# Optimization experiments

Measured on AMD Instinct MI355X. Metric: run time of the kernel, lower is better.

## Reference

```python
import jax, jax.numpy as jnp
import numpy as np

B, L, D_IN, H, N2, NL = 8, 4096, 128, 256, 8, 4  # d_state=16 -> N2=8 conjugate pairs


def setup_inputs() -> dict:
    key = jax.random.key(0)
    ks = jax.random.split(key, 10)
    x = jax.random.normal(ks[0], (B, L, D_IN), jnp.float32)
    enc_w = jax.random.normal(ks[1], (H, D_IN), jnp.float32) / np.float32(np.sqrt(D_IN))
    enc_b = jax.random.normal(ks[2], (H,), jnp.float32) * 0.01
    # S4D kernel params, stacked over NL layers
    log_dt = (jax.random.uniform(ks[3], (NL, H), jnp.float32)
              * np.float32(np.log(0.1) - np.log(0.001)) + np.float32(np.log(0.001)))
    log_A_real = jnp.full((NL, H, N2), np.float32(np.log(0.5)), jnp.float32)
    A_imag = jnp.ones((NL, H, 1), jnp.float32) * (np.pi * jnp.arange(N2, dtype=jnp.float32))
    C_re = jax.random.normal(ks[4], (NL, H, N2), jnp.float32) * np.float32(0.5 ** 0.5)
    C_im = jax.random.normal(ks[5], (NL, H, N2), jnp.float32) * np.float32(0.5 ** 0.5)
    D_skip = jax.random.normal(ks[6], (NL, H), jnp.float32)
    out_w = jax.random.normal(ks[7], (NL, 2 * H, H), jnp.float32) / np.float32(np.sqrt(H))
    out_b = jnp.zeros((NL, 2 * H), jnp.float32)
    return {"x": x, "enc_w": enc_w, "enc_b": enc_b, "log_dt": log_dt,
            "log_A_real": log_A_real, "A_imag": A_imag, "C_re": C_re, "C_im": C_im,
            "D_skip": D_skip, "out_w": out_w, "out_b": out_b}


def _s4d_layer(z, log_dt, log_A_real, A_imag, C_re, C_im, D_skip, out_w, out_b):
    # z: (B, L, H) -> u: (B, H, L)
    u = jnp.swapaxes(z, 1, 2)
    Lq = u.shape[-1]
    dt = jnp.exp(log_dt)                       # (H,)
    A = -jnp.exp(log_A_real) + 1j * A_imag     # (H, N2) complex
    dtA = A * dt[:, None]                      # (H, N2)
    Ck = (C_re + 1j * C_im) * (jnp.exp(dtA) - 1.0) / A  # ZOH discretization of C
    # Vandermonde kernel: K[h,l] = 2*Re(sum_n Ck[h,n] * exp(dtA[h,n]*l))
    t = jnp.arange(Lq, dtype=jnp.float32)
    K = 2.0 * jnp.einsum('hn,hnl->hl', Ck, jnp.exp(dtA[:, :, None] * t)).real  # (H, L)
    # FFT circular conv on 2L grid -> causal linear conv
    n_fft = 2 * Lq
    y = jnp.fft.irfft(jnp.fft.rfft(u, n=n_fft) * jnp.fft.rfft(K, n=n_fft), n=n_fft)[..., :Lq]
    y = y + u * D_skip[:, None]                # skip connection
    y = jax.nn.gelu(y)                         # final_act='gelu'
    y = jnp.einsum('bhl,ph->bpl', y, out_w) + out_b[None, :, None]  # 1x1 conv H->2H
    a, g = jnp.split(y, 2, axis=1)
    y = a * jax.nn.sigmoid(g)                  # GLU
    return jnp.swapaxes(y, 1, 2)               # (B, L, H)


def reference(x, enc_w, enc_b, log_dt, log_A_real, A_imag, C_re, C_im, D_skip, out_w, out_b):
    h = x @ enc_w.T + enc_b                    # encoder Linear: (B, L, H)
    for i in range(NL):                        # small fixed structural loop over layers
        z = _s4d_layer(h, log_dt[i], log_A_real[i], A_imag[i],
                       C_re[i], C_im[i], D_skip[i], out_w[i], out_b[i])
        h = z + h                              # residual (dropout=0 -> identity)
    return h
```

## Files before the change

### kernel.cpp

```cpp
#include <hip/hip_runtime.h>
#include <hip/hip_bf16.h>
#include <math.h>

#define Bn   8
#define Ln   4096
#define DINn 128
#define Hn   256
#define N2n  8
#define NLn  4

typedef __attribute__((ext_vector_type(4))) float f32x4;
typedef __attribute__((ext_vector_type(8))) short bf16x8;

__device__ __forceinline__ float gelu_f(float x) {
    float x2 = x * x;
    float inner = 0.7978845608028654f * x * fmaf(0.044715f, x2, 1.0f);
    float e = __expf(2.0f * inner);
    float th = 1.0f - 2.0f / (e + 1.0f);
    return 0.5f * x * (1.0f + th);
}

__device__ __forceinline__ float sigmoid_f(float x) {
    return 1.0f / (1.0f + __expf(-x));
}

__device__ __forceinline__ unsigned short f2bf(float f) {
    union { __hip_bfloat16 b; unsigned short u; } cv;
    cv.b = __float2bfloat16(f);
    return cv.u;
}

__device__ __forceinline__ uint4 pack8(float4 a, float4 b) {
    uint4 v;
    v.x = (unsigned)f2bf(a.x) | ((unsigned)f2bf(a.y) << 16);
    v.y = (unsigned)f2bf(a.z) | ((unsigned)f2bf(a.w) << 16);
    v.z = (unsigned)f2bf(b.x) | ((unsigned)f2bf(b.y) << 16);
    v.w = (unsigned)f2bf(b.z) | ((unsigned)f2bf(b.w) << 16);
    return v;
}

__global__ __launch_bounds__(256) void s4_scan_kernel(
    const float* __restrict__ hT,
    unsigned short* __restrict__ yT,
    const float* __restrict__ log_dt,
    const float* __restrict__ log_A_real,
    const float* __restrict__ A_imag,
    const float* __restrict__ C_re,
    const float* __restrict__ C_im,
    const float* __restrict__ D_skip)
{
    __shared__ float u_lds[4][64][65];
    const int tid = threadIdx.x;
    const int v = tid >> 6;
    const int t = tid & 63;
    const int h = blockIdx.x * 4 + v;
    const int b = blockIdx.y;

    const size_t rowbase = (size_t)(b * Hn + h) * Ln + (size_t)t * 64;
    const float* src = hT + rowbase;
    float* uL = &u_lds[v][t][0];

    #pragma unroll
    for (int j4 = 0; j4 < 16; ++j4) {
        float4 g = *(const float4*)(src + j4 * 4);
        uL[j4 * 4 + 0] = g.x; uL[j4 * 4 + 1] = g.y;
        uL[j4 * 4 + 2] = g.z; uL[j4 * 4 + 3] = g.w;
    }

    float dt = expf(log_dt[h]);
    float wr[N2n], wi[N2n], cr[N2n], ci[N2n];
    #pragma unroll
    for (int n = 0; n < N2n; ++n) {
        float lar = log_A_real[h * N2n + n];
        float aim = A_imag[h * N2n + n];
        float are = -expf(lar);
        float dre = are * dt, dimv = aim * dt;
        float mag = expf(dre);
        float s_, c_;
        sincosf(dimv, &s_, &c_);
        float w_re = mag * c_, w_im = mag * s_;
        wr[n] = w_re; wi[n] = w_im;
        float nre = w_re - 1.0f, nim = w_im;
        float inv = 1.0f / (are * are + aim * aim);
        float tre = (nre * are + nim * aim) * inv;
        float tim = (nim * are - nre * aim) * inv;
        float Cr = C_re[h * N2n + n], Ci = C_im[h * N2n + n];
        cr[n] = Cr * tre - Ci * tim;
        ci[n] = Cr * tim + Ci * tre;
    }
    const float Dsk = D_skip[h];

    float sr[N2n], si[N2n];
    #pragma unroll
    for (int n = 0; n < N2n; ++n) { sr[n] = 0.0f; si[n] = 0.0f; }
    #pragma unroll 4
    for (int j = 0; j < 64; ++j) {
        float u = uL[j];
        float acc = 0.0f;
        #pragma unroll
        for (int n = 0; n < N2n; ++n) {
            float nr = fmaf(wr[n], sr[n], fmaf(-wi[n], si[n], u));
            float ni = fmaf(wi[n], sr[n], wr[n] * si[n]);
            sr[n] = nr; si[n] = ni;
            acc = fmaf(cr[n], nr, fmaf(-ci[n], ni, acc));
        }
        uL[j] = fmaf(2.0f, acc, Dsk * u);
    }

    float mr[N2n], mi[N2n];
    #pragma unroll
    for (int n = 0; n < N2n; ++n) {
        float ar = wr[n], ai = wi[n];
        #pragma unroll
        for (int q = 0; q < 6; ++q) { float nr2 = ar * ar - ai * ai; ai = 2.0f * ar * ai; ar = nr2; }
        mr[n] = ar; mi[n] = ai;
    }
    for (int dlt = 1; dlt < 64; dlt <<= 1) {
        #pragma unroll
        for (int n = 0; n < N2n; ++n) {
            float tr = __shfl_up(sr[n], (unsigned)dlt, 64);
            float ti = __shfl_up(si[n], (unsigned)dlt, 64);
            float trz = (t >= dlt) ? tr : 0.0f;
            float tiz = (t >= dlt) ? ti : 0.0f;
            sr[n] = fmaf(mr[n], trz, fmaf(-mi[n], tiz, sr[n]));
            si[n] = fmaf(mr[n], tiz, fmaf(mi[n], trz, si[n]));
        }
        #pragma unroll
        for (int n = 0; n < N2n; ++n) {
            float nr2 = mr[n] * mr[n] - mi[n] * mi[n];
            mi[n] = 2.0f * mr[n] * mi[n];
            mr[n] = nr2;
        }
    }
    float pr[N2n], pim[N2n];
    #pragma unroll
    for (int n = 0; n < N2n; ++n) {
        float er = __shfl_up(sr[n], 1u, 64);
        float ei = __shfl_up(si[n], 1u, 64);
        pr[n]  = (t >= 1) ? er : 0.0f;
        pim[n] = (t >= 1) ? ei : 0.0f;
    }

    float dr2[N2n], di2[N2n];
    #pragma unroll
    for (int n = 0; n < N2n; ++n) { dr2[n] = cr[n]; di2[n] = ci[n]; }
    unsigned short* dst = yT + rowbase;
    for (int j8 = 0; j8 < 8; ++j8) {
        unsigned short rs[8];
        #pragma unroll
        for (int c = 0; c < 8; ++c) {
            float corr = 0.0f;
            #pragma unroll
            for (int n = 0; n < N2n; ++n) {
                float nr2 = dr2[n] * wr[n] - di2[n] * wi[n];
                float ni2 = dr2[n] * wi[n] + di2[n] * wr[n];
                dr2[n] = nr2; di2[n] = ni2;
                corr = fmaf(nr2, pr[n], fmaf(-ni2, pim[n], corr));
            }
            float yv = fmaf(2.0f, corr, uL[j8 * 8 + c]);
            rs[c] = f2bf(gelu_f(yv));
        }
        uint4 o;
        o.x = (unsigned)rs[0] | ((unsigned)rs[1] << 16);
        o.y = (unsigned)rs[2] | ((unsigned)rs[3] << 16);
        o.z = (unsigned)rs[4] | ((unsigned)rs[5] << 16);
        o.w = (unsigned)rs[6] | ((unsigned)rs[7] << 16);
        *(uint4*)(dst + j8 * 8) = o;
    }
}

template<int KDIM, bool GLU, bool ACVT, bool KMAJ, bool LAST>
__global__ __launch_bounds__(256) void mfma_gemm(
    const unsigned short* __restrict__ Abf,
    const float* __restrict__ Af,
    const float* __restrict__ W,
    const float* __restrict__ ba,
    const float* __restrict__ bg,
    float* hTbuf,
    float* Hout)
{
    constexpr int SM_MAIN = 128 * 72 * 2 + (GLU ? 2 : 1) * 64 * 72 * 2;
    constexpr int SM_TS = 64 * 132 * 4;
    constexpr int SM = SM_MAIN > SM_TS ? SM_MAIN : SM_TS;
    __shared__ __align__(16) char smem[SM];
    unsigned short* As  = (unsigned short*)smem;
    unsigned short* Bs0 = As + 128 * 72;
    unsigned short* Bs1 = Bs0 + 64 * 72;
    float* ts = (float*)smem;

    const int tid = threadIdx.x;
    const int lane = tid & 63, w = tid >> 6;
    const int wm = w >> 1, wn = w & 1;
    const int lr = lane & 15, lq = lane >> 4;
    const int row0 = blockIdx.x * 128;
    const int n0 = blockIdx.y * 64;
    const int bb = row0 >> 12;
    const int l0 = row0 & (Ln - 1);

    f32x4 accA[4][2], accG[4][2];
    #pragma unroll
    for (int i = 0; i < 4; ++i)
        #pragma unroll
        for (int j = 0; j < 2; ++j) {
            accA[i][j] = (f32x4)0.0f;
            if constexpr (GLU) accG[i][j] = (f32x4)0.0f;
        }

    for (int kt = 0; kt < KDIM / 64; ++kt) {
        const int k0 = kt * 64;
        if constexpr (ACVT) {
            #pragma unroll
            for (int it = 0; it < 4; ++it) {
                int idx = it * 256 + tid; int m = idx >> 3, q = idx & 7;
                const float* s = Af + (size_t)(row0 + m) * KDIM + k0 + q * 8;
                float4 g1 = *(const float4*)s;
                float4 g2 = *(const float4*)(s + 4);
                *(uint4*)(&As[m * 72 + q * 8]) = pack8(g1, g2);
            }
        } else {
            #pragma unroll
            for (int it = 0; it < 4; ++it) {
                int p = tid >> 2;
                int c = (tid & 3) | (it << 2);
                uint4 g = *(const uint4*)(Abf + (size_t)(bb * Hn + k0 + p) * Ln + l0 + c * 8);
                unsigned short* d = &As[(c * 8) * 72 + p];
                d[0 * 72] = g.x & 0xffff; d[1 * 72] = g.x >> 16;
                d[2 * 72] = g.y & 0xffff; d[3 * 72] = g.y >> 16;
                d[4 * 72] = g.z & 0xffff; d[5 * 72] = g.z >> 16;
                d[6 * 72] = g.w & 0xffff; d[7 * 72] = g.w >> 16;
            }
        }
        #pragma unroll
        for (int it = 0; it < 2; ++it) {
            int idx = it * 256 + tid; int p = idx >> 3, q = idx & 7;
            {
                const float* s = W + (size_t)(n0 + p) * KDIM + k0 + q * 8;
                float4 g1 = *(const float4*)s;
                float4 g2 = *(const float4*)(s + 4);
                *(uint4*)(&Bs0[p * 72 + q * 8]) = pack8(g1, g2);
            }
            if constexpr (GLU) {
                const float* s = W + (size_t)(256 + n0 + p) * KDIM + k0 + q * 8;
                float4 g1 = *(const float4*)s;
                float4 g2 = *(const float4*)(s + 4);
                *(uint4*)(&Bs1[p * 72 + q * 8]) = pack8(g1, g2);
            }
        }
        __syncthreads();
        #pragma unroll
        for (int kf = 0; kf < 2; ++kf) {
            bf16x8 av[4], bv[2], gv[2];
            #pragma unroll
            for (int mf = 0; mf < 4; ++mf)
                av[mf] = *(const bf16x8*)(&As[(wm * 64 + mf * 16 + lr) * 72 + (kf * 4 + lq) * 8]);
            #pragma unroll
            for (int nf = 0; nf < 2; ++nf) {
                bv[nf] = *(const bf16x8*)(&Bs0[(wn * 32 + nf * 16 + lr) * 72 + (kf * 4 + lq) * 8]);
                if constexpr (GLU)
                    gv[nf] = *(const bf16x8*)(&Bs1[(wn * 32 + nf * 16 + lr) * 72 + (kf * 4 + lq) * 8]);
            }
            #pragma unroll
            for (int mf = 0; mf < 4; ++mf)
                #pragma unroll
                for (int nf = 0; nf < 2; ++nf) {
                    accA[mf][nf] = __builtin_amdgcn_mfma_f32_16x16x32_bf16(av[mf], bv[nf], accA[mf][nf], 0, 0, 0);
                    if constexpr (GLU)
                        accG[mf][nf] = __builtin_amdgcn_mfma_f32_16x16x32_bf16(av[mf], gv[nf], accG[mf][nf], 0, 0, 0);
                }
        }
        __syncthreads();
    }

    float bA[2], bG[2];
    #pragma unroll
    for (int nf = 0; nf < 2; ++nf) {
        int pc = n0 + wn * 32 + nf * 16 + lr;
        bA[nf] = ba[pc];
        if constexpr (GLU) bG[nf] = bg[pc];
    }
    #pragma unroll
    for (int mf = 0; mf < 4; ++mf) {
        #pragma unroll
        for (int r = 0; r < 4; ++r) {
            int m_loc = wm * 64 + mf * 16 + lq * 4 + r;
            #pragma unroll
            for (int nf = 0; nf < 2; ++nf) {
                float val;
                if constexpr (GLU) {
                    float aval = accA[mf][nf][r] + bA[nf];
                    float gval = accG[mf][nf][r] + bG[nf];
                    val = aval * sigmoid_f(gval);
                } else {
                    val = accA[mf][nf][r] + bA[nf];
                }
                ts[(wn * 32 + nf * 16 + lr) * 132 + m_loc] = val;
            }
        }
    }
    __syncthreads();

    if constexpr (!LAST) {
        #pragma unroll
        for (int it2 = 0; it2 < 8; ++it2) {
            int idx = it2 * 256 + tid;
            int nn = idx >> 5, m4 = (idx & 31) * 4;
            float4 o = *(const float4*)(&ts[nn * 132 + m4]);
            float* gp = hTbuf + (size_t)(bb * Hn + n0 + nn) * Ln + l0 + m4;
            if constexpr (GLU) {
                float4 rr = *(const float4*)gp;
                o.x += rr.x; o.y += rr.y; o.z += rr.z; o.w += rr.w;
            }
            *(float4*)gp = o;
        }
    } else {
        #pragma unroll
        for (int it2 = 0; it2 < 8; ++it2) {
            int idx = it2 * 256 + tid;
            int nn = idx >> 5, m4 = (idx & 31) * 4;
            float4 o = *(const float4*)(&ts[nn * 132 + m4]);
            const float* gp = hTbuf + (size_t)(bb * Hn + n0 + nn) * Ln + l0 + m4;
            float4 rr = *(const float4*)gp;
            o.x += rr.x; o.y += rr.y; o.z += rr.z; o.w += rr.w;
            *(float4*)(&ts[nn * 132 + m4]) = o;
        }
        __syncthreads();
        #pragma unroll
        for (int it2 = 0; it2 < 8; ++it2) {
            int idx = it2 * 256 + tid;
            int m = idx >> 4, n4 = (idx & 15) * 4;
            float4 o;
            o.x = ts[(n4 + 0) * 132 + m];
            o.y = ts[(n4 + 1) * 132 + m];
            o.z = ts[(n4 + 2) * 132 + m];
            o.w = ts[(n4 + 3) * 132 + m];
            *(float4*)(Hout + (size_t)(row0 + m) * Hn + n0 + n4) = o;
        }
    }
}

extern "C" void kernel_launch(void* const* d_in, const int* in_sizes, int n_in,
                              void* d_out, int out_size, void* d_ws, size_t ws_size,
                              hipStream_t stream) {
    (void)in_sizes; (void)n_in; (void)out_size; (void)ws_size;
    const float* x          = (const float*)d_in[0];
    const float* enc_w      = (const float*)d_in[1];
    const float* enc_b      = (const float*)d_in[2];
    const float* log_dt     = (const float*)d_in[3];
    const float* log_A_real = (const float*)d_in[4];
    const float* A_imag     = (const float*)d_in[5];
    const float* C_re       = (const float*)d_in[6];
    const float* C_im       = (const float*)d_in[7];
    const float* D_skip     = (const float*)d_in[8];
    const float* out_w      = (const float*)d_in[9];
    const float* out_b      = (const float*)d_in[10];

    const size_t NE = (size_t)Bn * Hn * Ln;
    float* h  = (float*)d_out;
    float* hT = (float*)d_ws;
    unsigned short* yT = (unsigned short*)(hT + NE);

    const dim3 gg(256, 4), gb(256);

    mfma_gemm<DINn, false, true, false, false><<<gg, gb, 0, stream>>>(
        nullptr, x, enc_w, enc_b, nullptr, hT, nullptr);

    for (int i = 0; i < NLn; ++i) {
        s4_scan_kernel<<<dim3(Hn / 4, Bn), gb, 0, stream>>>(
            hT, yT,
            log_dt + (size_t)i * Hn,
            log_A_real + (size_t)i * Hn * N2n,
            A_imag + (size_t)i * Hn * N2n,
            C_re + (size_t)i * Hn * N2n,
            C_im + (size_t)i * Hn * N2n,
            D_skip + (size_t)i * Hn);
        const float* wlay = out_w + (size_t)i * 2 * Hn * Hn;
        const float* bl = out_b + (size_t)i * 2 * Hn;
        if (i == NLn - 1) {
            mfma_gemm<Hn, true, false, true, true><<<gg, gb, 0, stream>>>(
                yT, nullptr, wlay, bl, bl + Hn, hT, h);
        } else {
            mfma_gemm<Hn, true, false, true, false><<<gg, gb, 0, stream>>>(
                yT, nullptr, wlay, bl, bl + Hn, hT, nullptr);
        }
    }
}
```

Baseline: 286.8 us.

## Split each scan row across two wavefronts with cross-wave state carry

```diff
diff --git a/kernel.cpp b/kernel.cpp
--- a/kernel.cpp
+++ b/kernel.cpp
@@ -39,7 +39,7 @@
     return v;
 }
 
-__global__ __launch_bounds__(256) void s4_scan_kernel(
+__global__ __launch_bounds__(256, 4) void s4_scan_kernel(
     const float* __restrict__ hT,
     unsigned short* __restrict__ yT,
     const float* __restrict__ log_dt,
@@ -49,19 +49,23 @@
     const float* __restrict__ C_im,
     const float* __restrict__ D_skip)
 {
-    __shared__ float u_lds[4][64][65];
+    __shared__ float u_lds[2][128][33];
+    __shared__ float Sbuf[2][16];
+
     const int tid = threadIdx.x;
-    const int v = tid >> 6;
+    const int w = tid >> 6;
     const int t = tid & 63;
-    const int h = blockIdx.x * 4 + v;
+    const int rowloc = w >> 1;
+    const int half = w & 1;
+    const int h = blockIdx.x * 2 + rowloc;
     const int b = blockIdx.y;
 
-    const size_t rowbase = (size_t)(b * Hn + h) * Ln + (size_t)t * 64;
+    const size_t rowbase = (size_t)(b * Hn + h) * Ln + (size_t)half * 2048 + (size_t)t * 32;
     const float* src = hT + rowbase;
-    float* uL = &u_lds[v][t][0];
-
-    #pragma unroll
-    for (int j4 = 0; j4 < 16; ++j4) {
+    float* uL = &u_lds[rowloc][half * 64 + t][0];
+
+    #pragma unroll
+    for (int j4 = 0; j4 < 8; ++j4) {
         float4 g = *(const float4*)(src + j4 * 4);
         uL[j4 * 4 + 0] = g.x; uL[j4 * 4 + 1] = g.y;
         uL[j4 * 4 + 2] = g.z; uL[j4 * 4 + 3] = g.w;
@@ -94,7 +98,7 @@
     #pragma unroll
     for (int n = 0; n < N2n; ++n) { sr[n] = 0.0f; si[n] = 0.0f; }
     #pragma unroll 4
-    for (int j = 0; j < 64; ++j) {
+    for (int j = 0; j < 32; ++j) {
         float u = uL[j];
         float acc = 0.0f;
         #pragma unroll
@@ -107,14 +111,16 @@
         uL[j] = fmaf(2.0f, acc, Dsk * u);
     }
 
-    float mr[N2n], mi[N2n];
+    float mr[N2n], mi[N2n], ar[N2n], ai[N2n];
     #pragma unroll
     for (int n = 0; n < N2n; ++n) {
-        float ar = wr[n], ai = wi[n];
-        #pragma unroll
-        for (int q = 0; q < 6; ++q) { float nr2 = ar * ar - ai * ai; ai = 2.0f * ar * ai; ar = nr2; }
-        mr[n] = ar; mi[n] = ai;
-    }
+        float br = wr[n], bi = wi[n];
+        #pragma unroll
+        for (int q = 0; q < 5; ++q) { float nr2 = br * br - bi * bi; bi = 2.0f * br * bi; br = nr2; }
+        mr[n] = br; mi[n] = bi;
+        ar[n] = 1.0f; ai[n] = 0.0f;
+    }
+    #pragma unroll
     for (int dlt = 1; dlt < 64; dlt <<= 1) {
         #pragma unroll
         for (int n = 0; n < N2n; ++n) {
@@ -124,12 +130,22 @@
             float tiz = (t >= dlt) ? ti : 0.0f;
             sr[n] = fmaf(mr[n], trz, fmaf(-mi[n], tiz, sr[n]));
             si[n] = fmaf(mr[n], tiz, fmaf(mi[n], trz, si[n]));
-        }
-        #pragma unroll
-        for (int n = 0; n < N2n; ++n) {
+            float nar = ar[n] * mr[n] - ai[n] * mi[n];
+            float nai = ar[n] * mi[n] + ai[n] * mr[n];
+            bool bit = (t & dlt) != 0;
+            ar[n] = bit ? nar : ar[n];
+            ai[n] = bit ? nai : ai[n];
             float nr2 = mr[n] * mr[n] - mi[n] * mi[n];
             mi[n] = 2.0f * mr[n] * mi[n];
             mr[n] = nr2;
+        }
+    }
+
+    if (half == 0 && t == 63) {
+        #pragma unroll
+        for (int n = 0; n < N2n; ++n) {
+            Sbuf[rowloc][2 * n] = sr[n];
+            Sbuf[rowloc][2 * n + 1] = si[n];
         }
     }
     float pr[N2n], pim[N2n];
@@ -140,12 +156,21 @@
         pr[n]  = (t >= 1) ? er : 0.0f;
         pim[n] = (t >= 1) ? ei : 0.0f;
     }
+    __syncthreads();
+    if (half == 1) {
+        #pragma unroll
+        for (int n = 0; n < N2n; ++n) {
+            float SAr = Sbuf[rowloc][2 * n], SAi = Sbuf[rowloc][2 * n + 1];
+            pr[n]  = fmaf(ar[n], SAr, fmaf(-ai[n], SAi, pr[n]));
+            pim[n] = fmaf(ar[n], SAi, fmaf(ai[n], SAr, pim[n]));
+        }
+    }
 
     float dr2[N2n], di2[N2n];
     #pragma unroll
     for (int n = 0; n < N2n; ++n) { dr2[n] = cr[n]; di2[n] = ci[n]; }
     unsigned short* dst = yT + rowbase;
-    for (int j8 = 0; j8 < 8; ++j8) {
+    for (int j8 = 0; j8 < 4; ++j8) {
         unsigned short rs[8];
         #pragma unroll
         for (int c = 0; c < 8; ++c) {
@@ -365,7 +390,7 @@
         nullptr, x, enc_w, enc_b, nullptr, hT, nullptr);
 
     for (int i = 0; i < NLn; ++i) {
-        s4_scan_kernel<<<dim3(Hn / 4, Bn), gb, 0, stream>>>(
+        s4_scan_kernel<<<dim3(Hn / 2, Bn), gb, 0, stream>>>(
             hT, yT,
             log_dt + (size_t)i * Hn,
             log_A_real + (size_t)i * Hn * N2n,
```

Measured after the change: 453.9 us. +58.3%, slower.
